# Kernel tuning notes

Measured on AMD Instinct MI355X. Metric: run time of the kernel, lower is better.

Reference implementation:

```python
import jax, jax.numpy as jnp
import numpy as np

N = 100000   # nodes
B = 64       # graphs in batch
E = 1600000  # edges
D_IN = 2
W1D = W2D = W3D = 128
N_CLASSES = 3
MIN_SCORE = 0.1
TOL = 1e-7
BN_EPS = 1e-5


def setup_inputs() -> dict:
    key = jax.random.key(0)
    ks = jax.random.split(key, 32)
    inp = {}
    inp['x'] = jax.random.normal(ks[0], (N, D_IN), jnp.float32)
    inp['edge_index'] = jax.random.randint(ks[1], (2, E), 0, N, dtype=jnp.int32)
    inp['batch_index'] = jnp.sort(jax.random.randint(ks[2], (N,), 0, B, dtype=jnp.int32))
    inp['topk_w'] = jax.random.normal(ks[3], (D_IN,), jnp.float32)
    dims = [(D_IN, W1D), (W1D, W2D), (W2D, W3D)]
    k = 4
    for i, (din, dout) in enumerate(dims, start=1):
        inp[f'W{i}'] = jax.random.normal(ks[k], (din, dout), jnp.float32) * (1.0 / np.sqrt(din)); k += 1
        inp[f'b{i}'] = jax.random.normal(ks[k], (dout,), jnp.float32) * 0.05; k += 1
        inp[f'g{i}'] = 1.0 + 0.1 * jax.random.normal(ks[k], (dout,), jnp.float32); k += 1
        inp[f'be{i}'] = 0.1 * jax.random.normal(ks[k], (dout,), jnp.float32); k += 1
        inp[f'rm{i}'] = 0.1 * jax.random.normal(ks[k], (dout,), jnp.float32); k += 1
        inp[f'rv{i}'] = 1.0 + 0.1 * jax.random.uniform(ks[k], (dout,), jnp.float32); k += 1
    inp['linW'] = jax.random.normal(ks[k], (W3D, N_CLASSES), jnp.float32) * (1.0 / np.sqrt(W3D)); k += 1
    inp['linb'] = jax.random.normal(ks[k], (N_CLASSES,), jnp.float32) * 0.05
    return inp


def _bn_eval(x, g, be, rm, rv):
    # BatchNorm1d in eval mode (running stats)
    return (x - rm) * jax.lax.rsqrt(rv + BN_EPS) * g + be


def _gcn(x, src, dst, ew, W, b):
    # GCNConv: lin -> symmetric-normalized scatter-add (self-loops already in src/dst/ew)
    xw = x @ W                                   # [N, dout]
    deg = jax.ops.segment_sum(ew, dst, num_segments=N)
    dinv = jnp.where(deg > 0, jax.lax.rsqrt(deg), 0.0)
    norm = dinv[src] * ew * dinv[dst]            # [E+N]
    out = jax.ops.segment_sum(norm[:, None] * xw[src], dst, num_segments=N)
    return out + b


def reference(x, edge_index, batch_index, topk_w,
              W1, b1, g1, be1, rm1, rv1,
              W2, b2, g2, be2, rm2, rv2,
              W3, b3, g3, be3, rm3, rv3,
              linW, linb):
    # ---- TopKPooling (min_score mode): per-graph softmax score, threshold keep,
    # x scaled by score. Implemented via masking (fixed shapes): dropped nodes get
    # zero features, zero edge weights, and -inf at the max pool -> math identical
    # to PyG's node filtering (BN is eval-mode, i.e. per-node).
    logits = x @ topk_w                                                    # [N]
    m = jax.ops.segment_max(logits, batch_index, num_segments=B)
    e = jnp.exp(logits - m[batch_index])
    score = e / jax.ops.segment_sum(e, batch_index, num_segments=B)[batch_index]
    smax = jax.ops.segment_max(score, batch_index, num_segments=B)[batch_index] - TOL
    keep = score > jnp.minimum(smax, MIN_SCORE)                            # [N] bool
    keep_f = keep.astype(x.dtype)
    h = x * (score * keep_f)[:, None]

    src0, dst0 = edge_index[0], edge_index[1]
    loop = jnp.arange(N, dtype=src0.dtype)
    src = jnp.concatenate([src0, loop])
    dst = jnp.concatenate([dst0, loop])
    ew = jnp.concatenate([keep_f[src0] * keep_f[dst0], keep_f])            # mask + self-loops

    h = _bn_eval(jax.nn.relu(_gcn(h, src, dst, ew, W1, b1)), g1, be1, rm1, rv1)
    h = _bn_eval(jax.nn.relu(_gcn(h, src, dst, ew, W2, b2)), g2, be2, rm2, rv2)
    h = _bn_eval(jax.nn.relu(_gcn(h, src, dst, ew, W3, b3)), g3, be3, rm3, rv3)

    neg = jnp.finfo(h.dtype).min
    h = jnp.where(keep[:, None], h, neg)
    pooled = jax.ops.segment_max(h, batch_index, num_segments=B)           # [B, w3]
    out = pooled @ linW + linb
    return jax.nn.log_softmax(out, axis=1)
```

## Files before the change

### kernel.cpp

```cpp
#include <hip/hip_runtime.h>

#define NN 100000
#define BB 64
#define EE 1600000
#define FD 128
#define SLOTC 64
#define KSLOTS (BB * SLOTC)
#define EMAXE (1 << 20)
#define LCAP 12288

__global__ __launch_bounds__(256) void k_scorekeep(
    const float2* __restrict__ x, const int* __restrict__ bidx,
    const float* __restrict__ tw,
    unsigned char* __restrict__ kf, int* __restrict__ nslot,
    int* __restrict__ knt, float* __restrict__ degs,
    float2* __restrict__ h0s, int* __restrict__ kecnt)
{
    __shared__ float cache[LCAP];
    __shared__ float red[256];
    __shared__ int   klist[SLOTC];
    __shared__ int   lcnt;
    __shared__ float shv;
    int b = blockIdx.x, tid = threadIdx.x;
    if (tid == 0) { lcnt = 0; if (b == 0) *kecnt = 0; }

    int lo = 0, hi = NN;
    while (lo < hi) { int mid = (lo + hi) >> 1; if (bidx[mid] < b) lo = mid + 1; else hi = mid; }
    int s0 = lo;
    hi = NN;
    while (lo < hi) { int mid = (lo + hi) >> 1; if (bidx[mid] < b + 1) lo = mid + 1; else hi = mid; }
    int L = lo - s0;
    float w0 = tw[0], w1 = tw[1];
    bool fit = (L <= LCAP);
    __syncthreads();

    float mx = -3.4028235e38f;
    for (int j = tid; j < L; j += 256) {
        float2 v = x[s0 + j];
        float l = v.x * w0 + v.y * w1;
        if (fit) cache[j] = l;
        kf[s0 + j] = 0;
        mx = fmaxf(mx, l);
    }
    red[tid] = mx; __syncthreads();
    for (int s = 128; s > 0; s >>= 1) { if (tid < s) red[tid] = fmaxf(red[tid], red[tid + s]); __syncthreads(); }
    if (tid == 0) shv = red[0];
    __syncthreads();
    float m = shv;

    float sm = 0.f;
    for (int j = tid; j < L; j += 256) {
        float l;
        if (fit) l = cache[j];
        else { float2 v = x[s0 + j]; l = v.x * w0 + v.y * w1; }
        float e = expf(l - m);
        if (fit) cache[j] = e;
        sm += e;
    }
    red[tid] = sm; __syncthreads();
    for (int s = 128; s > 0; s >>= 1) { if (tid < s) red[tid] += red[tid + s]; __syncthreads(); }
    if (tid == 0) shv = red[0];
    __syncthreads();
    float S = shv;

    float smx = -3.4028235e38f;
    for (int j = tid; j < L; j += 256) {
        float e;
        if (fit) e = cache[j];
        else { float2 v = x[s0 + j]; e = expf(v.x * w0 + v.y * w1 - m); }
        float sc = e / S;
        if (fit) cache[j] = sc;
        smx = fmaxf(smx, sc);
    }
    red[tid] = smx; __syncthreads();
    for (int s = 128; s > 0; s >>= 1) { if (tid < s) red[tid] = fmaxf(red[tid], red[tid + s]); __syncthreads(); }
    if (tid == 0) shv = fminf(red[0] - 1e-7f, 0.1f);
    __syncthreads();
    float thr = shv;

    for (int j = tid; j < L; j += 256) {
        float sc;
        if (fit) sc = cache[j];
        else { float2 v = x[s0 + j]; sc = expf(v.x * w0 + v.y * w1 - m) / S; }
        if (sc > thr) {
            int l = atomicAdd(&lcnt, 1);
            if (l < SLOTC) klist[l] = j;
        }
    }
    __syncthreads();
    int nk = lcnt; if (nk > SLOTC) nk = SLOTC;
    if (tid == 0) knt[b] = nk;
    for (int l = tid; l < nk; l += 256) {
        int j = klist[l], i = s0 + j;
        float sc;
        if (fit) sc = cache[j];
        else { float2 v = x[i]; sc = expf(v.x * w0 + v.y * w1 - m) / S; }
        int slot = b * SLOTC + l;
        kf[i] = 1; nslot[i] = slot;
        degs[slot] = 1.0f;
        float2 v = x[i];
        h0s[slot] = make_float2(v.x * sc, v.y * sc);
    }
}

__global__ void k_edges(const int* __restrict__ ei, const unsigned char* __restrict__ kf,
                        const int* __restrict__ nslot, float* __restrict__ degs,
                        int* __restrict__ kedge, int* __restrict__ kecnt) {
    int e = blockIdx.x * 256 + threadIdx.x;
    if (e >= EE) return;
    int s = ei[e];
    if (kf[s]) {
        int d = ei[EE + e];
        if (kf[d]) {
            int ds = nslot[d];
            atomicAdd(&degs[ds], 1.0f);
            int idx = atomicAdd(kecnt, 1);
            if (idx < EMAXE) { kedge[2 * idx] = nslot[s]; kedge[2 * idx + 1] = ds; }
        }
    }
}

__global__ __launch_bounds__(256) void k_tail1(
    const float* __restrict__ degs, const float2* __restrict__ h0s,
    const int* __restrict__ kedge, const int* __restrict__ kecnt,
    const int* __restrict__ knt,
    const float* __restrict__ W1, const float* __restrict__ b1,
    const float* __restrict__ g1, const float* __restrict__ be1,
    const float* __restrict__ rm1, const float* __restrict__ rv1,
    const float* __restrict__ W2, float* __restrict__ hY)
{
    __shared__ float ftile[SLOTC * FD];
    __shared__ float2 psl[SLOTC];
    __shared__ int keS, nkS;
    int b = blockIdx.x, tid = threadIdx.x;
    if (tid == 0) { int k = *kecnt; keS = k > EMAXE ? EMAXE : k; nkS = knt[b]; }
    for (int j = tid; j < SLOTC; j += 256) psl[j] = make_float2(0.f, 0.f);
    __syncthreads();
    int ke = keS, nk = nkS;
    for (int t = tid; t < ke; t += 256) {
        int d = kedge[2 * t + 1];
        if ((d >> 6) == b) {
            int s = kedge[2 * t], ld = d & 63;
            float nm = rsqrtf(degs[s]) * rsqrtf(degs[d]);
            float2 h = h0s[s];
            atomicAdd(&psl[ld].x, nm * h.x);
            atomicAdd(&psl[ld].y, nm * h.y);
        }
    }
    __syncthreads();
    for (int j = tid; j < nk * FD; j += 256) {
        int ld = j >> 7, f = j & 127, slot = b * SLOTC + ld;
        float di = rsqrtf(degs[slot]), d2 = di * di;
        float2 h = h0s[slot];
        float a0 = psl[ld].x + d2 * h.x;
        float a1 = psl[ld].y + d2 * h.y;
        float v = a0 * W1[f] + a1 * W1[FD + f] + b1[f];
        v = fmaxf(v, 0.f);
        v = (v - rm1[f]) * rsqrtf(rv1[f] + 1e-5f) * g1[f] + be1[f];
        ftile[j] = v;
    }
    __syncthreads();
    for (int j = tid; j < nk * FD; j += 256) {
        int ld = j >> 7, f = j & 127;
        const float* xr = ftile + ld * FD;
        float acc = 0.f;
        #pragma unroll 8
        for (int k = 0; k < FD; k++) acc += xr[k] * W2[k * FD + f];
        hY[(b * SLOTC + ld) * FD + f] = acc;
    }
}

__global__ __launch_bounds__(256) void k_tail2(
    const float* __restrict__ degs, const int* __restrict__ kedge,
    const int* __restrict__ kecnt, const int* __restrict__ knt,
    const float* __restrict__ hY,
    const float* __restrict__ b2, const float* __restrict__ g2,
    const float* __restrict__ be2, const float* __restrict__ rm2,
    const float* __restrict__ rv2,
    const float* __restrict__ W3, float* __restrict__ hYB)
{
    __shared__ float ftile[SLOTC * FD];
    __shared__ int keS, nkS;
    int b = blockIdx.x, tid = threadIdx.x;
    if (tid == 0) { int k = *kecnt; keS = k > EMAXE ? EMAXE : k; nkS = knt[b]; }
    __syncthreads();
    int ke = keS, nk = nkS;
    for (int j = tid; j < nk * FD; j += 256) ftile[j] = 0.f;
    __syncthreads();
    for (long long idx = tid; idx < (long long)ke * FD; idx += 256) {
        int e = (int)(idx >> 7), f = (int)(idx & 127);
        int d = kedge[2 * e + 1];
        if ((d >> 6) == b) {
            int s = kedge[2 * e];
            float nm = rsqrtf(degs[s]) * rsqrtf(degs[d]);
            atomicAdd(&ftile[(d & 63) * FD + f], nm * hY[s * FD + f]);
        }
    }
    __syncthreads();
    for (int j = tid; j < nk * FD; j += 256) {
        int ld = j >> 7, f = j & 127, slot = b * SLOTC + ld;
        float di = rsqrtf(degs[slot]);
        float v = ftile[j] + di * di * hY[slot * FD + f] + b2[f];
        v = fmaxf(v, 0.f);
        v = (v - rm2[f]) * rsqrtf(rv2[f] + 1e-5f) * g2[f] + be2[f];
        ftile[j] = v;
    }
    __syncthreads();
    for (int j = tid; j < nk * FD; j += 256) {
        int ld = j >> 7, f = j & 127;
        const float* xr = ftile + ld * FD;
        float acc = 0.f;
        #pragma unroll 8
        for (int k = 0; k < FD; k++) acc += xr[k] * W3[k * FD + f];
        hYB[(b * SLOTC + ld) * FD + f] = acc;
    }
}

__global__ __launch_bounds__(256) void k_tail3(
    const float* __restrict__ degs, const int* __restrict__ kedge,
    const int* __restrict__ kecnt, const int* __restrict__ knt,
    const float* __restrict__ hYB,
    const float* __restrict__ b3, const float* __restrict__ g3,
    const float* __restrict__ be3, const float* __restrict__ rm3,
    const float* __restrict__ rv3,
    const float* __restrict__ linW, const float* __restrict__ linb,
    float* __restrict__ out)
{
    __shared__ float ftile[SLOTC * FD];
    __shared__ float poolv[FD];
    __shared__ int keS, nkS;
    int b = blockIdx.x, tid = threadIdx.x;
    if (tid == 0) { int k = *kecnt; keS = k > EMAXE ? EMAXE : k; nkS = knt[b]; }
    __syncthreads();
    int ke = keS, nk = nkS;
    for (int j = tid; j < nk * FD; j += 256) ftile[j] = 0.f;
    __syncthreads();
    for (long long idx = tid; idx < (long long)ke * FD; idx += 256) {
        int e = (int)(idx >> 7), f = (int)(idx & 127);
        int d = kedge[2 * e + 1];
        if ((d >> 6) == b) {
            int s = kedge[2 * e];
            float nm = rsqrtf(degs[s]) * rsqrtf(degs[d]);
            atomicAdd(&ftile[(d & 63) * FD + f], nm * hYB[s * FD + f]);
        }
    }
    __syncthreads();
    for (int j = tid; j < nk * FD; j += 256) {
        int ld = j >> 7, f = j & 127, slot = b * SLOTC + ld;
        float di = rsqrtf(degs[slot]);
        float v = ftile[j] + di * di * hYB[slot * FD + f] + b3[f];
        v = fmaxf(v, 0.f);
        v = (v - rm3[f]) * rsqrtf(rv3[f] + 1e-5f) * g3[f] + be3[f];
        ftile[j] = v;
    }
    __syncthreads();
    for (int f = tid; f < FD; f += 256) {
        float mx = -3.4028235e38f;
        for (int ld = 0; ld < nk; ld++) mx = fmaxf(mx, ftile[ld * FD + f]);
        poolv[f] = mx;
    }
    __syncthreads();
    if (tid == 0) {
        float z0 = linb[0], z1 = linb[1], z2 = linb[2];
        for (int f = 0; f < FD; f++) {
            float pv = poolv[f];
            z0 += pv * linW[f * 3 + 0];
            z1 += pv * linW[f * 3 + 1];
            z2 += pv * linW[f * 3 + 2];
        }
        float m = fmaxf(z0, fmaxf(z1, z2));
        float l = m + logf(expf(z0 - m) + expf(z1 - m) + expf(z2 - m));
        out[b * 3 + 0] = z0 - l;
        out[b * 3 + 1] = z1 - l;
        out[b * 3 + 2] = z2 - l;
    }
}

extern "C" void kernel_launch(void* const* d_in, const int* in_sizes, int n_in,
                              void* d_out, int out_size, void* d_ws, size_t ws_size,
                              hipStream_t stream) {
    (void)in_sizes; (void)n_in; (void)out_size; (void)ws_size;
    const float* x    = (const float*)d_in[0];
    const int*   ei   = (const int*)d_in[1];
    const int*   bidx = (const int*)d_in[2];
    const float* tw   = (const float*)d_in[3];
    const float* W1 = (const float*)d_in[4],  *b1 = (const float*)d_in[5],  *g1 = (const float*)d_in[6];
    const float* be1= (const float*)d_in[7],  *rm1= (const float*)d_in[8],  *rv1= (const float*)d_in[9];
    const float* W2 = (const float*)d_in[10], *b2 = (const float*)d_in[11], *g2 = (const float*)d_in[12];
    const float* be2= (const float*)d_in[13], *rm2= (const float*)d_in[14], *rv2= (const float*)d_in[15];
    const float* W3 = (const float*)d_in[16], *b3 = (const float*)d_in[17], *g3 = (const float*)d_in[18];
    const float* be3= (const float*)d_in[19], *rm3= (const float*)d_in[20], *rv3= (const float*)d_in[21];
    const float* linW = (const float*)d_in[22], *linb = (const float*)d_in[23];
    float* out = (float*)d_out;

    char* w = (char*)d_ws;
    auto take = [&](size_t bytes) { char* r = w; w += (bytes + 255) & ~(size_t)255; return r; };
    int*   kecnt = (int*)take(16);
    int*   knt   = (int*)take((size_t)BB * 4);
    unsigned char* kf = (unsigned char*)take(NN);
    int*   nslot = (int*)take((size_t)NN * 4);
    float* degs  = (float*)take((size_t)KSLOTS * 4);
    float2* h0s  = (float2*)take((size_t)KSLOTS * 8);
    int*   kedge = (int*)take((size_t)EMAXE * 8);
    float* hY    = (float*)take((size_t)KSLOTS * FD * 4);
    float* hYB   = (float*)take((size_t)KSLOTS * FD * 4);

    k_scorekeep<<<BB, 256, 0, stream>>>((const float2*)x, bidx, tw, kf, nslot, knt, degs, h0s, kecnt);
    k_edges<<<(EE + 255) / 256, 256, 0, stream>>>(ei, kf, nslot, degs, kedge, kecnt);
    k_tail1<<<BB, 256, 0, stream>>>(degs, h0s, kedge, kecnt, knt,
                                    W1, b1, g1, be1, rm1, rv1, W2, hY);
    k_tail2<<<BB, 256, 0, stream>>>(degs, kedge, kecnt, knt, hY,
                                    b2, g2, be2, rm2, rv2, W3, hYB);
    k_tail3<<<BB, 256, 0, stream>>>(degs, kedge, kecnt, knt, hYB,
                                    b3, g3, be3, rm3, rv3, linW, linb, out);
}
```

Baseline: 149.4 us.

## Use keep bitmask, precomputed graph starts, and vectorized edge filtering

Adds a kernel that computes per-graph start offsets from the sorted batch index and clears a keep bitmask, replacing the per-block binary searches. The score kernel drops its shared-memory cache and the max-score reduction, deriving the threshold analytically as 1/S (the max softmax value), and recomputes exp on each pass instead. The keep flags become a 100k-bit bitmask, small enough to stay cache-resident for the random lookups in edge filtering, and edge sources are read as int4 with four edges per thread. It adds one kernel launch and relies on the max score being exactly 1/S up to rounding.

```diff
diff --git a/kernel.cpp b/kernel.cpp
--- a/kernel.cpp
+++ b/kernel.cpp
@@ -7,40 +7,46 @@
 #define SLOTC 64
 #define KSLOTS (BB * SLOTC)
 #define EMAXE (1 << 20)
-#define LCAP 12288
+#define NWORDS ((NN + 31) / 32)
+
+__global__ void k_starts(const int* __restrict__ bidx, int* __restrict__ starts,
+                         unsigned* __restrict__ kfbits, int* __restrict__ kecnt) {
+    int gt = blockIdx.x * 256 + threadIdx.x, G = gridDim.x * 256;
+    if (gt == 0) *kecnt = 0;
+    for (int i = gt; i <= NN; i += G) {
+        if (i == 0) {
+            int c = bidx[0];
+            for (int v = 0; v <= c; v++) starts[v] = 0;
+        } else if (i == NN) {
+            int a = bidx[NN - 1];
+            for (int v = a + 1; v <= BB; v++) starts[v] = NN;
+        } else {
+            int a = bidx[i - 1], c = bidx[i];
+            for (int v = a + 1; v <= c; v++) starts[v] = i;
+        }
+    }
+    for (int w = gt; w < NWORDS; w += G) kfbits[w] = 0u;
+}
 
 __global__ __launch_bounds__(256) void k_scorekeep(
-    const float2* __restrict__ x, const int* __restrict__ bidx,
+    const float2* __restrict__ x, const int* __restrict__ starts,
     const float* __restrict__ tw,
-    unsigned char* __restrict__ kf, int* __restrict__ nslot,
-    int* __restrict__ knt, float* __restrict__ degs,
-    float2* __restrict__ h0s, int* __restrict__ kecnt)
+    unsigned* __restrict__ kfbits, int* __restrict__ nslot,
+    int* __restrict__ knt, float* __restrict__ degs, float2* __restrict__ h0s)
 {
-    __shared__ float cache[LCAP];
     __shared__ float red[256];
     __shared__ int   klist[SLOTC];
     __shared__ int   lcnt;
     __shared__ float shv;
     int b = blockIdx.x, tid = threadIdx.x;
-    if (tid == 0) { lcnt = 0; if (b == 0) *kecnt = 0; }
-
-    int lo = 0, hi = NN;
-    while (lo < hi) { int mid = (lo + hi) >> 1; if (bidx[mid] < b) lo = mid + 1; else hi = mid; }
-    int s0 = lo;
-    hi = NN;
-    while (lo < hi) { int mid = (lo + hi) >> 1; if (bidx[mid] < b + 1) lo = mid + 1; else hi = mid; }
-    int L = lo - s0;
+    if (tid == 0) lcnt = 0;
+    int s0 = starts[b], e0 = starts[b + 1], L = e0 - s0;
     float w0 = tw[0], w1 = tw[1];
-    bool fit = (L <= LCAP);
-    __syncthreads();
 
     float mx = -3.4028235e38f;
     for (int j = tid; j < L; j += 256) {
         float2 v = x[s0 + j];
-        float l = v.x * w0 + v.y * w1;
-        if (fit) cache[j] = l;
-        kf[s0 + j] = 0;
-        mx = fmaxf(mx, l);
+        mx = fmaxf(mx, v.x * w0 + v.y * w1);
     }
     red[tid] = mx; __syncthreads();
     for (int s = 128; s > 0; s >>= 1) { if (tid < s) red[tid] = fmaxf(red[tid], red[tid + s]); __syncthreads(); }
@@ -50,38 +56,19 @@
 
     float sm = 0.f;
     for (int j = tid; j < L; j += 256) {
-        float l;
-        if (fit) l = cache[j];
-        else { float2 v = x[s0 + j]; l = v.x * w0 + v.y * w1; }
-        float e = expf(l - m);
-        if (fit) cache[j] = e;
-        sm += e;
+        float2 v = x[s0 + j];
+        sm += expf(v.x * w0 + v.y * w1 - m);
     }
     red[tid] = sm; __syncthreads();
     for (int s = 128; s > 0; s >>= 1) { if (tid < s) red[tid] += red[tid + s]; __syncthreads(); }
     if (tid == 0) shv = red[0];
     __syncthreads();
     float S = shv;
-
-    float smx = -3.4028235e38f;
+    float thr = fminf(1.0f / S - 1e-7f, 0.1f);
+
     for (int j = tid; j < L; j += 256) {
-        float e;
-        if (fit) e = cache[j];
-        else { float2 v = x[s0 + j]; e = expf(v.x * w0 + v.y * w1 - m); }
-        float sc = e / S;
-        if (fit) cache[j] = sc;
-        smx = fmaxf(smx, sc);
-    }
-    red[tid] = smx; __syncthreads();
-    for (int s = 128; s > 0; s >>= 1) { if (tid < s) red[tid] = fmaxf(red[tid], red[tid + s]); __syncthreads(); }
-    if (tid == 0) shv = fminf(red[0] - 1e-7f, 0.1f);
-    __syncthreads();
-    float thr = shv;
-
-    for (int j = tid; j < L; j += 256) {
-        float sc;
-        if (fit) sc = cache[j];
-        else { float2 v = x[s0 + j]; sc = expf(v.x * w0 + v.y * w1 - m) / S; }
+        float2 v = x[s0 + j];
+        float sc = expf(v.x * w0 + v.y * w1 - m) / S;
         if (sc > thr) {
             int l = atomicAdd(&lcnt, 1);
             if (l < SLOTC) klist[l] = j;
@@ -91,31 +78,36 @@
     int nk = lcnt; if (nk > SLOTC) nk = SLOTC;
     if (tid == 0) knt[b] = nk;
     for (int l = tid; l < nk; l += 256) {
-        int j = klist[l], i = s0 + j;
-        float sc;
-        if (fit) sc = cache[j];
-        else { float2 v = x[i]; sc = expf(v.x * w0 + v.y * w1 - m) / S; }
+        int i = s0 + klist[l];
+        float2 v = x[i];
+        float sc = expf(v.x * w0 + v.y * w1 - m) / S;
         int slot = b * SLOTC + l;
-        kf[i] = 1; nslot[i] = slot;
+        atomicOr(&kfbits[i >> 5], 1u << (i & 31));
+        nslot[i] = slot;
         degs[slot] = 1.0f;
-        float2 v = x[i];
         h0s[slot] = make_float2(v.x * sc, v.y * sc);
     }
 }
 
-__global__ void k_edges(const int* __restrict__ ei, const unsigned char* __restrict__ kf,
-                        const int* __restrict__ nslot, float* __restrict__ degs,
-                        int* __restrict__ kedge, int* __restrict__ kecnt) {
-    int e = blockIdx.x * 256 + threadIdx.x;
-    if (e >= EE) return;
-    int s = ei[e];
-    if (kf[s]) {
-        int d = ei[EE + e];
-        if (kf[d]) {
-            int ds = nslot[d];
-            atomicAdd(&degs[ds], 1.0f);
-            int idx = atomicAdd(kecnt, 1);
-            if (idx < EMAXE) { kedge[2 * idx] = nslot[s]; kedge[2 * idx + 1] = ds; }
+__global__ void k_edges(const int4* __restrict__ src4, const int* __restrict__ ei,
+                        const unsigned* __restrict__ kfbits, const int* __restrict__ nslot,
+                        float* __restrict__ degs, int* __restrict__ kedge,
+                        int* __restrict__ kecnt) {
+    int t = blockIdx.x * 256 + threadIdx.x;
+    if (t * 4 >= EE) return;
+    int4 s4 = src4[t];
+    int ss[4] = {s4.x, s4.y, s4.z, s4.w};
+    #pragma unroll
+    for (int q = 0; q < 4; q++) {
+        int s = ss[q];
+        if ((kfbits[s >> 5] >> (s & 31)) & 1u) {
+            int d = ei[EE + t * 4 + q];
+            if ((kfbits[d >> 5] >> (d & 31)) & 1u) {
+                int ds = nslot[d];
+                atomicAdd(&degs[ds], 1.0f);
+                int idx = atomicAdd(kecnt, 1);
+                if (idx < EMAXE) { kedge[2 * idx] = nslot[s]; kedge[2 * idx + 1] = ds; }
+            }
         }
     }
 }
@@ -295,18 +287,22 @@
 
     char* w = (char*)d_ws;
     auto take = [&](size_t bytes) { char* r = w; w += (bytes + 255) & ~(size_t)255; return r; };
-    int*   kecnt = (int*)take(16);
-    int*   knt   = (int*)take((size_t)BB * 4);
-    unsigned char* kf = (unsigned char*)take(NN);
-    int*   nslot = (int*)take((size_t)NN * 4);
-    float* degs  = (float*)take((size_t)KSLOTS * 4);
-    float2* h0s  = (float2*)take((size_t)KSLOTS * 8);
-    int*   kedge = (int*)take((size_t)EMAXE * 8);
-    float* hY    = (float*)take((size_t)KSLOTS * FD * 4);
-    float* hYB   = (float*)take((size_t)KSLOTS * FD * 4);
-
-    k_scorekeep<<<BB, 256, 0, stream>>>((const float2*)x, bidx, tw, kf, nslot, knt, degs, h0s, kecnt);
-    k_edges<<<(EE + 255) / 256, 256, 0, stream>>>(ei, kf, nslot, degs, kedge, kecnt);
+    int*      kecnt  = (int*)take(16);
+    int*      starts = (int*)take((size_t)(BB + 1) * 4);
+    int*      knt    = (int*)take((size_t)BB * 4);
+    unsigned* kfbits = (unsigned*)take((size_t)NWORDS * 4);
+    int*      nslot  = (int*)take((size_t)NN * 4);
+    float*    degs   = (float*)take((size_t)KSLOTS * 4);
+    float2*   h0s    = (float2*)take((size_t)KSLOTS * 8);
+    int*      kedge  = (int*)take((size_t)EMAXE * 8);
+    float*    hY     = (float*)take((size_t)KSLOTS * FD * 4);
+    float*    hYB    = (float*)take((size_t)KSLOTS * FD * 4);
+
+    k_starts<<<392, 256, 0, stream>>>(bidx, starts, kfbits, kecnt);
+    k_scorekeep<<<BB, 256, 0, stream>>>((const float2*)x, starts, tw,
+                                        kfbits, nslot, knt, degs, h0s);
+    k_edges<<<(EE / 4 + 255) / 256, 256, 0, stream>>>((const int4*)ei, ei, kfbits,
+                                                      nslot, degs, kedge, kecnt);
     k_tail1<<<BB, 256, 0, stream>>>(degs, h0s, kedge, kecnt, knt,
                                     W1, b1, g1, be1, rm1, rv1, W2, hY);
     k_tail2<<<BB, 256, 0, stream>>>(degs, kedge, kecnt, knt, hY,
```

New measurement: 142.8 us. 1.05x faster.
